# Optimization experiments

Measured on AMD Instinct MI355X. Metric: run time of the kernel, lower is better.

The kernel has to match this reference:

```python
import jax, jax.numpy as jnp
import numpy as np

B, LQ, LK, E, H, NF, NE, HID = 4, 8192, 8192, 256, 8, 2, 4, 256


def _split(x, h):
    b, l, e = x.shape
    return x.reshape(b, l, h, e // h).transpose(0, 2, 1, 3)  # (B,H,L,D)


def _merge(x):
    b, h, l, d = x.shape
    return x.transpose(0, 2, 1, 3).reshape(b, l, h * d)


def _experts(x, W1, b1, W2, b2, W3, b3):
    # x: (B,N,in); W*: (E, out, in). Returns (E,B,N,out). Exact (erf) GELU as torch.
    h = jax.nn.gelu(jnp.einsum('bni,ehi->ebnh', x, W1) + b1[:, None, None, :], approximate=False)
    h = jax.nn.gelu(jnp.einsum('ebnh,egh->ebng', h, W2) + b2[:, None, None, :], approximate=False)
    return jnp.einsum('ebng,eog->ebno', h, W3) + b3[:, None, None, :]


def _combine(expert_out, scores):
    # expert_out: (E,B,N,out); scores: (B,N,1,E) -> (B,N,out)
    return jnp.einsum('ebno,bne->bno', expert_out, scores[:, :, 0, :])


def _forward(scores, query, input_functions,
             ca_Wq, ca_bq, ca_Wk, ca_bk, ca_Wv, ca_bv, ca_Wo, ca_bo,
             sa_Wq, sa_bq, sa_Wk, sa_bk, sa_Wv, sa_bv, sa_Wo, sa_bo,
             f1_W1, f1_b1, f1_W2, f1_b2, f1_W3, f1_b3,
             f2_W1, f2_b1, f2_W2, f2_b2, f2_W3, f2_b3):
    h = H
    # ---- cross attention over NF input functions ----
    q = jax.nn.softmax(_split(query @ ca_Wq.T + ca_bq, h), -1)  # (B,H,Lq,D)
    k = jnp.einsum('fble,fde->fbld', input_functions, ca_Wk) + ca_bk[:, None, None, :]
    v = jnp.einsum('fble,fde->fbld', input_functions, ca_Wv) + ca_bv[:, None, None, :]
    f, b, lk, e = k.shape
    d = e // h
    k = jax.nn.softmax(k.reshape(f, b, lk, h, d).transpose(0, 1, 3, 2, 4), -1)  # (F,B,H,Lk,D)
    v = v.reshape(f, b, lk, h, d).transpose(0, 1, 3, 2, 4)
    k_sum = k.sum(3, keepdims=True)                       # (F,B,H,1,D)
    alpha = 1.0 / (q[None] * k_sum).sum(-1, keepdims=True)  # (F,B,H,Lq,1)
    tmp = jnp.einsum('fbhld,fbhlv->fbhdv', k, v)          # (F,B,H,D,D)
    out = (alpha * jnp.einsum('bhld,fbhdv->fbhlv', q, tmp)).mean(0)  # (B,H,Lq,D)
    ca = (_merge(q) + _merge(out)) @ ca_Wo.T + ca_bo
    # expert FFN1 + score-weighted combine, residual
    query = query + _combine(_experts(ca, f1_W1, f1_b1, f1_W2, f1_b2, f1_W3, f1_b3), scores)
    # ---- self attention ----
    q2 = jax.nn.softmax(_split(query @ sa_Wq.T + sa_bq, h), -1)
    k2 = jax.nn.softmax(_split(query @ sa_Wk.T + sa_bk, h), -1)
    v2 = _split(query @ sa_Wv.T + sa_bv, h)
    k_sum2 = k2.sum(2, keepdims=True)
    alpha2 = 1.0 / (q2 * k_sum2).sum(-1, keepdims=True)
    tmp2 = jnp.einsum('bhld,bhlv->bhdv', k2, v2)
    out2 = alpha2 * jnp.einsum('bhld,bhdv->bhlv', q2, tmp2)
    sa = (_merge(q2) + _merge(out2)) @ sa_Wo.T + sa_bo
    query = query + _combine(_experts(sa, f2_W1, f2_b1, f2_W2, f2_b2, f2_W3, f2_b3), scores)
    return query


def setup_inputs() -> dict:
    ks = iter(jax.random.split(jax.random.key(0), 64))
    def p(shape):
        return jax.random.normal(next(ks), shape, jnp.float32) * 0.02
    inp = {
        'scores': jax.random.uniform(next(ks), (B, LQ, 1, NE), jnp.float32),
        'query': jax.random.normal(next(ks), (B, LQ, E), jnp.float32),
        'input_functions': jax.random.normal(next(ks), (NF, B, LK, E), jnp.float32),
        'ca_Wq': p((E, E)), 'ca_bq': p((E,)),
        'ca_Wk': p((NF, E, E)), 'ca_bk': p((NF, E)),
        'ca_Wv': p((NF, E, E)), 'ca_bv': p((NF, E)),
        'ca_Wo': p((E, E)), 'ca_bo': p((E,)),
        'sa_Wq': p((E, E)), 'sa_bq': p((E,)),
        'sa_Wk': p((E, E)), 'sa_bk': p((E,)),
        'sa_Wv': p((E, E)), 'sa_bv': p((E,)),
        'sa_Wo': p((E, E)), 'sa_bo': p((E,)),
        'f1_W1': p((NE, HID, E)), 'f1_b1': p((NE, HID)),
        'f1_W2': p((NE, HID, HID)), 'f1_b2': p((NE, HID)),
        'f1_W3': p((NE, HID, HID)), 'f1_b3': p((NE, HID)),
        'f2_W1': p((NE, HID, E)), 'f2_b1': p((NE, HID)),
        'f2_W2': p((NE, HID, HID)), 'f2_b2': p((NE, HID)),
        'f2_W3': p((NE, HID, HID)), 'f2_b3': p((NE, HID)),
    }
    return inp


def reference(scores, query, input_functions,
              ca_Wq, ca_bq, ca_Wk, ca_bk, ca_Wv, ca_bv, ca_Wo, ca_bo,
              sa_Wq, sa_bq, sa_Wk, sa_bk, sa_Wv, sa_bv, sa_Wo, sa_bo,
              f1_W1, f1_b1, f1_W2, f1_b2, f1_W3, f1_b3,
              f2_W1, f2_b1, f2_W2, f2_b2, f2_W3, f2_b3):
    return _forward(scores, query, input_functions,
                    ca_Wq, ca_bq, ca_Wk, ca_bk, ca_Wv, ca_bv, ca_Wo, ca_bo,
                    sa_Wq, sa_bq, sa_Wk, sa_bk, sa_Wv, sa_bv, sa_Wo, sa_bo,
                    f1_W1, f1_b1, f1_W2, f1_b2, f1_W3, f1_b3,
                    f2_W1, f2_b1, f2_W2, f2_b2, f2_W3, f2_b3)
```

## Files before the change

kernel.cpp:

```cpp
#include <hip/hip_runtime.h>


typedef unsigned short u16;
typedef __attribute__((ext_vector_type(8))) short   bs8;
typedef __attribute__((ext_vector_type(4))) float   f32x4;
typedef __attribute__((ext_vector_type(16))) float  f32x16;

__device__ __forceinline__ float bf2f(u16 u) {
  union { float f; unsigned i; } c; c.i = ((unsigned)u) << 16; return c.f;
}
__device__ __forceinline__ u16 f2bf(float f) {
  union { float f; unsigned i; } c; c.f = f;
  unsigned x = c.i;
  return (u16)((x + 0x7fffu + ((x >> 16) & 1u)) >> 16);
}
__device__ __forceinline__ unsigned pack2(float a, float b) {
  return (unsigned)f2bf(a) | ((unsigned)f2bf(b) << 16);
}
__device__ __forceinline__ float gelu_f(float x) {
  const float t = x * (0.7978845608f + 0.0356774081f * x * x);
  return x * __builtin_amdgcn_rcpf(1.f + __expf(-2.f * t));
}

#define EPI_PLAIN 0
#define EPI_QSM   4

template <bool AF32, int EPI>
__global__ __launch_bounds__(256, 2) void gemm256(
    const void* __restrict__ Ain, const u16* __restrict__ W,
    const float* __restrict__ bias, u16* __restrict__ outb) {
  __shared__ int4 ash[1024];
  __shared__ int4 wsh[1024];
  const int tid = threadIdx.x;
  const int m0 = blockIdx.x * 128, n0 = blockIdx.y * 128;
  const int wave = tid >> 6, lane = tid & 63;
  const int wm = (wave >> 1) * 64, wn = (wave & 1) * 64;
  const int lr = lane & 15, lk = lane >> 4;
  f32x4 acc[4][4];
#pragma unroll
  for (int m = 0; m < 4; ++m)
#pragma unroll
    for (int n = 0; n < 4; ++n) acc[m][n] = f32x4{0.f, 0.f, 0.f, 0.f};

  const float* Af = (const float*)Ain;
  const u16*   Ab = (const u16*)Ain;

  for (int kt = 0; kt < 4; ++kt) {
    const int k0 = kt * 64;
    if (kt) __syncthreads();
#pragma unroll
    for (int it = 0; it < 4; ++it) {
      const int s = tid + it * 256;
      const int row = s >> 3, c16 = s & 7;
      const int dst = (row << 3) | (c16 ^ (row & 7));
      const long src = (long)(m0 + row) * 256 + k0 + c16 * 8;
      int4 val;
      if constexpr (AF32) {
        const float4* p = (const float4*)(Af + src);
        const float4 x = p[0], y = p[1];
        val.x = pack2(x.x, x.y); val.y = pack2(x.z, x.w);
        val.z = pack2(y.x, y.y); val.w = pack2(y.z, y.w);
      } else {
        val = *(const int4*)(Ab + src);
      }
      ash[dst] = val;
    }
#pragma unroll
    for (int it = 0; it < 4; ++it) {
      const int s = tid + it * 256;
      const int row = s >> 3, c16 = s & 7;
      const int dst = (row << 3) | (c16 ^ (row & 7));
      wsh[dst] = *(const int4*)(W + (long)(n0 + row) * 256 + k0 + c16 * 8);
    }
    __syncthreads();
#pragma unroll
    for (int kk = 0; kk < 2; ++kk) {
      bs8 af[4], wf[4];
#pragma unroll
      for (int m = 0; m < 4; ++m) {
        const int row = wm + m * 16 + lr;
        af[m] = *(const bs8*)&ash[(row << 3) | ((kk * 4 + lk) ^ (row & 7))];
      }
#pragma unroll
      for (int n = 0; n < 4; ++n) {
        const int row = wn + n * 16 + lr;
        wf[n] = *(const bs8*)&wsh[(row << 3) | ((kk * 4 + lk) ^ (row & 7))];
      }
#pragma unroll
      for (int m = 0; m < 4; ++m)
#pragma unroll
        for (int n = 0; n < 4; ++n)
          acc[m][n] = __builtin_amdgcn_mfma_f32_16x16x32_bf16(af[m], wf[n],
                                                              acc[m][n], 0, 0, 0);
    }
  }
  if constexpr (EPI == EPI_QSM) {
#pragma unroll
    for (int m = 0; m < 4; ++m) {
      const int rb = m0 + wm + m * 16 + lk * 4;
#pragma unroll
      for (int j = 0; j < 4; ++j) {
#pragma unroll
        for (int hh = 0; hh < 2; ++hh) {
          const int c0 = n0 + wn + (2 * hh) * 16 + lr;
          const float p0 = __expf(acc[m][2 * hh][j] + bias[c0]);
          const float p1 = __expf(acc[m][2 * hh + 1][j] + bias[c0 + 16]);
          float s = p0 + p1;
#pragma unroll
          for (int o = 8; o >= 1; o >>= 1) s += __shfl_xor(s, o);
          const float inv = 1.0f / s;
          outb[(long)(rb + j) * 256 + c0]      = f2bf(p0 * inv);
          outb[(long)(rb + j) * 256 + c0 + 16] = f2bf(p1 * inv);
        }
      }
    }
  } else {
#pragma unroll
    for (int m = 0; m < 4; ++m) {
      const int rb = m0 + wm + m * 16 + lk * 4;
#pragma unroll
      for (int n = 0; n < 4; ++n) {
        const int gc = n0 + wn + n * 16 + lr;
        const float bv = bias[gc];
#pragma unroll
        for (int j = 0; j < 4; ++j)
          outb[(long)(rb + j) * 256 + gc] = f2bf(acc[m][n][j] + bv);
      }
    }
  }
}

__global__ __launch_bounds__(1024, 4) void ffn4(
    const u16* __restrict__ X, const u16* __restrict__ WX, int wbase,
    const float* __restrict__ b1, const float* __restrict__ b2,
    const float* __restrict__ b3, const float* __restrict__ scores,
    const float* __restrict__ csrc, float* __restrict__ outf) {
  __shared__ int4 xsh[2048];
  __shared__ int4 hsh[2048];
  const int tid = threadIdx.x, wave = tid >> 6, lane = tid & 63;
  const int wm = (wave >> 3) * 32;
  const int wn8 = wave & 7;
  const int lr = lane & 15, lk = lane >> 4;
  const long m0 = (long)blockIdx.x * 64;

#pragma unroll
  for (int it = 0; it < 2; ++it) {
    const int s = tid + it * 1024;
    const int row = s >> 5, c8 = s & 31;
    const int cs = (c8 & 24) | ((c8 ^ row) & 7);
    xsh[row * 32 + cs] = *(const int4*)(X + (m0 + row) * 256 + c8 * 8);
  }
  __syncthreads();

  f32x4 oacc[2][2];
#pragma unroll
  for (int m = 0; m < 2; ++m)
#pragma unroll
    for (int n = 0; n < 2; ++n) oacc[m][n] = f32x4{0.f, 0.f, 0.f, 0.f};
  f32x4 acc[2][2];

  for (int e = 0; e < 4; ++e) {
#pragma unroll 1
    for (int l = 0; l < 3; ++l) {
      const u16* wp = WX + (long)(wbase + l * 4 + e) * 65536 + (long)lane * 8;
      const int4* asrc = (l == 0) ? xsh : hsh;
#pragma unroll
      for (int m = 0; m < 2; ++m)
#pragma unroll
        for (int n = 0; n < 2; ++n) acc[m][n] = f32x4{0.f, 0.f, 0.f, 0.f};
#pragma unroll
      for (int kt = 0; kt < 8; ++kt) {
        bs8 af[2], wf[2];
        const int c8 = kt * 4 + lk;
#pragma unroll
        for (int m = 0; m < 2; ++m) {
          const int row = wm + m * 16 + lr;
          const int cs = (c8 & 24) | ((c8 ^ row) & 7);
          af[m] = *(const bs8*)&asrc[row * 32 + cs];
        }
#pragma unroll
        for (int n = 0; n < 2; ++n)
          wf[n] = *(const bs8*)(wp + ((kt * 16 + wn8 * 2 + n) << 9));
        __builtin_amdgcn_s_setprio(1);
#pragma unroll
        for (int m = 0; m < 2; ++m)
#pragma unroll
          for (int n = 0; n < 2; ++n)
            acc[m][n] = __builtin_amdgcn_mfma_f32_16x16x32_bf16(
                af[m], wf[n], acc[m][n], 0, 0, 0);
        __builtin_amdgcn_s_setprio(0);
      }
      if (l < 2) {
        __syncthreads();
        const float* bb = (l == 0 ? b1 : b2) + e * 256;
        u16* hp = (u16*)hsh;
#pragma unroll
        for (int m = 0; m < 2; ++m)
#pragma unroll
          for (int n = 0; n < 2; ++n) {
            const int col = wn8 * 32 + n * 16 + lr;
            const float bv = bb[col];
            const int c8w = col >> 3;
#pragma unroll
            for (int j = 0; j < 4; ++j) {
              const int row = wm + m * 16 + lk * 4 + j;
              const int cs = (c8w & 24) | ((c8w ^ row) & 7);
              hp[row * 256 + cs * 8 + (col & 7)] =
                  f2bf(gelu_f(acc[m][n][j] + bv));
            }
          }
        __syncthreads();
      } else {
#pragma unroll
        for (int m = 0; m < 2; ++m) {
#pragma unroll
          for (int j = 0; j < 4; ++j) {
            const float sc = scores[(m0 + wm + m * 16 + lk * 4 + j) * 4 + e];
#pragma unroll
            for (int n = 0; n < 2; ++n)
              oacc[m][n][j] +=
                  sc * (acc[m][n][j] + b3[e * 256 + wn8 * 32 + n * 16 + lr]);
          }
        }
      }
    }
  }
#pragma unroll
  for (int m = 0; m < 2; ++m) {
#pragma unroll
    for (int n = 0; n < 2; ++n) {
      const int col = wn8 * 32 + n * 16 + lr;
#pragma unroll
      for (int j = 0; j < 4; ++j) {
        const long idx = (m0 + wm + m * 16 + lk * 4 + j) * 256 + col;
        outf[idx] = csrc[idx] + oacc[m][n][j];
      }
    }
  }
}

__global__ __launch_bounds__(1024, 4) void kvstats(
    const float* __restrict__ Ain, const u16* __restrict__ Wk,
    const u16* __restrict__ Wv, const float* __restrict__ bk,
    const float* __restrict__ bv, float* __restrict__ pks,
    float* __restrict__ ptm) {
  __shared__ __align__(16) char smem[73728];
  int4* ash  = (int4*)smem;
  int4* wksh = ash + 512;
  int4* wvsh = wksh + 2048;
  u16* KnT = (u16*)smem;
  u16* VT  = KnT + 256 * 72;
  const int tid = threadIdx.x;
  const int wave = tid >> 6, lane = tid & 63;
  const int lr = lane & 15, lk = lane >> 4;
  const int kvsel = wave >> 3, w3 = wave & 7;
  const int wm = (w3 >> 2) * 32, wn = (w3 & 3) * 64;
  const int b = blockIdx.y, ch = blockIdx.x;
  const long r0 = (long)b * 8192 + (long)ch * 64;

  f32x4 acc[2][4];
#pragma unroll
  for (int m = 0; m < 2; ++m)
#pragma unroll
    for (int n = 0; n < 4; ++n) acc[m][n] = f32x4{0.f, 0.f, 0.f, 0.f};

  for (int kt = 0; kt < 4; ++kt) {
    const int k0 = kt * 64;
    if (kt) __syncthreads();
    if (tid < 512) {
      const int row = tid >> 3, c16 = tid & 7;
      const int dst = (row << 3) | (c16 ^ (row & 7));
      const float4* p = (const float4*)(Ain + (r0 + row) * 256 + k0 + c16 * 8);
      const float4 x = p[0], y = p[1];
      int4 val;
      val.x = pack2(x.x, x.y); val.y = pack2(x.z, x.w);
      val.z = pack2(y.x, y.y); val.w = pack2(y.z, y.w);
      ash[dst] = val;
    }
#pragma unroll
    for (int it = 0; it < 2; ++it) {
      const int s = tid + it * 1024;
      const int row = s >> 3, c16 = s & 7;
      const int dst = (row << 3) | (c16 ^ (row & 7));
      wksh[dst] = *(const int4*)(Wk + (long)row * 256 + k0 + c16 * 8);
      wvsh[dst] = *(const int4*)(Wv + (long)row * 256 + k0 + c16 * 8);
    }
    __syncthreads();
    const int4* wsh = kvsel ? wvsh : wksh;
#pragma unroll
    for (int kk = 0; kk < 2; ++kk) {
      bs8 af[2], wf[4];
#pragma unroll
      for (int m = 0; m < 2; ++m) {
        const int row = wm + m * 16 + lr;
        af[m] = *(const bs8*)&ash[(row << 3) | ((kk * 4 + lk) ^ (row & 7))];
      }
#pragma unroll
      for (int n = 0; n < 4; ++n) {
        const int row = wn + n * 16 + lr;
        wf[n] = *(const bs8*)&wsh[(row << 3) | ((kk * 4 + lk) ^ (row & 7))];
      }
#pragma unroll
      for (int m = 0; m < 2; ++m)
#pragma unroll
        for (int n = 0; n < 4; ++n)
          acc[m][n] = __builtin_amdgcn_mfma_f32_16x16x32_bf16(af[m], wf[n],
                                                              acc[m][n], 0, 0, 0);
    }
  }
  __syncthreads();

  const float* bias = kvsel ? bv : bk;
  if (kvsel == 0) {
#pragma unroll
    for (int m = 0; m < 2; ++m)
#pragma unroll
      for (int j = 0; j < 4; ++j)
#pragma unroll
        for (int hh = 0; hh < 2; ++hh) {
          const int c0 = wn + (2 * hh) * 16 + lr;
          const float p0 = __expf(acc[m][2 * hh][j] + bias[c0]);
          const float p1 = __expf(acc[m][2 * hh + 1][j] + bias[c0 + 16]);
          float s = p0 + p1;
#pragma unroll
          for (int o = 8; o >= 1; o >>= 1) s += __shfl_xor(s, o);
          const float inv = 1.0f / s;
          acc[m][2 * hh][j] = p0 * inv;
          acc[m][2 * hh + 1][j] = p1 * inv;
        }
  }
  {
    u16* T = kvsel ? VT : KnT;
#pragma unroll
    for (int m = 0; m < 2; ++m) {
      const int rb = wm + m * 16 + lk * 4;
#pragma unroll
      for (int n = 0; n < 4; ++n) {
        const int col = wn + n * 16 + lr;
        float v0 = acc[m][n][0], v1 = acc[m][n][1];
        float v2 = acc[m][n][2], v3 = acc[m][n][3];
        if (kvsel) {
          const float bb = bias[col];
          v0 += bb; v1 += bb; v2 += bb; v3 += bb;
        }
        uint2 w;
        w.x = pack2(v0, v1); w.y = pack2(v2, v3);
        *(uint2*)(T + col * 72 + rb) = w;
      }
    }
  }
  __syncthreads();

  if (kvsel == 0) {
    const int h = w3;
    f32x16 aT, aK;
#pragma unroll
    for (int r = 0; r < 16; ++r) { aT[r] = 0.f; aK[r] = 0.f; }
    bs8 ones;
#pragma unroll
    for (int e = 0; e < 8; ++e) ones[e] = (short)0x3F80;
    const u16* kcol = KnT + (h * 32 + (lane & 31)) * 72;
    const u16* vcol = VT  + (h * 32 + (lane & 31)) * 72;
    const int hi8 = (lane >> 5) * 8;
#pragma unroll
    for (int ks = 0; ks < 4; ++ks) {
      const bs8 a  = *(const bs8*)(kcol + ks * 16 + hi8);
      const bs8 vb = *(const bs8*)(vcol + ks * 16 + hi8);
      aT = __builtin_amdgcn_mfma_f32_32x32x16_bf16(vb, a, aT, 0, 0, 0);
      aK = __builtin_amdgcn_mfma_f32_32x32x16_bf16(a, ones, aK, 0, 0, 0);
    }
    const long blk = (long)b * gridDim.x + ch;
    float* po = ptm + blk * 8192 + h * 1024;
#pragma unroll
    for (int r = 0; r < 16; ++r) {
      const int dv = (r & 3) + 8 * (r >> 2) + 4 * (lane >> 5);
      po[dv * 32 + (lane & 31)] = aT[r];
    }
    if ((lane & 31) == 0) {
#pragma unroll
      for (int r = 0; r < 16; ++r) {
        const int dk = (r & 3) + 8 * (r >> 2) + 4 * (lane >> 5);
        pks[blk * 256 + h * 32 + dk] = aK[r];
      }
    }
  }
}

__global__ void reduceStats(const float* __restrict__ pk,
                            const float* __restrict__ pt,
                            float* __restrict__ ksum, float* __restrict__ tmp) {
  const int b = blockIdx.y;
  const int i = blockIdx.x * 256 + threadIdx.x;
  float s = 0.f;
  if (i < 256) {
    const float* p = pk + (long)b * 128 * 256 + i;
    for (int c = 0; c < 128; ++c) s += p[c * 256];
    ksum[(long)b * 256 + i] = s;
  } else {
    const int j = i - 256;
    const float* p = pt + (long)b * 128 * 8192 + j;
    for (int c = 0; c < 128; ++c) s += p[c * 8192];
    tmp[(long)b * 8192 + j] = s;
  }
}

template <int F>
__global__ __launch_bounds__(256, 2) void mixk(const u16* __restrict__ q,
                                               const float* __restrict__ ksum,
                                               const float* __restrict__ tmp,
                                               u16* __restrict__ out) {
  constexpr int LF = (F == 2) ? 1 : 0;
  constexpr int QS = 264;
  __shared__ u16 qsh[64 * QS];
  __shared__ float alsh[64][17];
  __shared__ float ksh[8][F * 36];
  const int t = threadIdx.x;
  const int h = t >> 5, dv = t & 31;
  const int b = blockIdx.y;
  const long row0 = (long)b * 8192 + (long)blockIdx.x * 64;

#pragma unroll
  for (int it = 0; it < 8; ++it) {
    const int i = t + it * 256;
    const int r = i >> 5, c = i & 31;
    *(int4*)&qsh[r * QS + c * 8] = *(const int4*)&q[(row0 + r) * 256 + c * 8];
  }
#pragma unroll
  for (int f = 0; f < F; ++f)
    ksh[h][f * 36 + dv] = ksum[((long)f * 4 + b) * 256 + t];
  float tr[F][32];
#pragma unroll
  for (int f = 0; f < F; ++f) {
    const float* tp = tmp + ((long)f * 4 + b) * 8192 + h * 1024 + dv * 32;
#pragma unroll
    for (int c = 0; c < 8; ++c) {
      const float4 v = *(const float4*)(tp + c * 4);
      tr[f][c * 4] = v.x; tr[f][c * 4 + 1] = v.y;
      tr[f][c * 4 + 2] = v.z; tr[f][c * 4 + 3] = v.w;
    }
  }
  __syncthreads();

  for (int d = t; d < 64 * 8 * F; d += 256) {
    const int f = d & (F - 1);
    const int hh = (d >> LF) & 7;
    const int r = d >> (3 + LF);
    const u16* qp = &qsh[r * QS + hh * 32];
    const float* kp = &ksh[hh][f * 36];
    float s = 0.f;
#pragma unroll
    for (int c = 0; c < 4; ++c) {
      const bs8 qa = *(const bs8*)(qp + c * 8);
#pragma unroll
      for (int j = 0; j < 8; ++j) s += bf2f((u16)qa[j]) * kp[c * 8 + j];
    }
    alsh[r][(hh << LF) | f] = 1.0f / s;
  }
  __syncthreads();

#pragma unroll 2
  for (int r = 0; r < 64; ++r) {
    float qr[32];
    const u16* qp = &qsh[r * QS + h * 32];
#pragma unroll
    for (int c = 0; c < 4; ++c) {
      const bs8 qa = *(const bs8*)(qp + c * 8);
#pragma unroll
      for (int j = 0; j < 8; ++j) qr[c * 8 + j] = bf2f((u16)qa[j]);
    }
    float acc = 0.f;
#pragma unroll
    for (int f = 0; f < F; ++f) {
      float s0 = 0.f, s1 = 0.f;
#pragma unroll
      for (int dk = 0; dk < 32; dk += 2) {
        s0 += qr[dk] * tr[f][dk];
        s1 += qr[dk + 1] * tr[f][dk + 1];
      }
      acc += (s0 + s1) * alsh[r][(h << LF) | f];
    }
    const float qv = bf2f(qsh[r * QS + t]);
    out[(row0 + r) * 256 + t] = f2bf(qv + acc * (1.0f / (float)F));
  }
}

struct WTab10 { const float* p[10]; };
__global__ void convW(WTab10 tab, u16* __restrict__ dst) {
  const int s = blockIdx.y;
  const long i = ((long)blockIdx.x * 256 + threadIdx.x) * 4;
  const float4 v = *(const float4*)(tab.p[s] + i);
  ushort4 o;
  o.x = f2bf(v.x); o.y = f2bf(v.y); o.z = f2bf(v.z); o.w = f2bf(v.w);
  *(ushort4*)(dst + (long)s * 65536 + i) = o;
}

struct WTab24 { const float* p[24]; };
__global__ void convWX(WTab24 tab, u16* __restrict__ dst) {
  const int s = blockIdx.y;
  const int o8 = blockIdx.x * 256 + threadIdx.x;
  const int kt = o8 >> 10, nt = (o8 >> 6) & 15, lane = o8 & 63;
  const int row = nt * 16 + (lane & 15);
  const int col = kt * 32 + (lane >> 4) * 8;
  const float* src = tab.p[s] + row * 256 + col;
  const float4 a = *(const float4*)src;
  const float4 b = *(const float4*)(src + 4);
  int4 val;
  val.x = pack2(a.x, a.y); val.y = pack2(a.z, a.w);
  val.z = pack2(b.x, b.y); val.w = pack2(b.z, b.w);
  *(int4*)(dst + (long)s * 65536 + (long)o8 * 8) = val;
}

extern "C" void kernel_launch(void* const* d_in, const int* in_sizes, int n_in,
                              void* d_out, int out_size, void* d_ws, size_t ws_size,
                              hipStream_t stream) {
  (void)in_sizes; (void)n_in; (void)out_size; (void)ws_size;
  const float* scores = (const float*)d_in[0];
  const float* query  = (const float*)d_in[1];
  const float* IF     = (const float*)d_in[2];
  const float* ca_Wq = (const float*)d_in[3];  const float* ca_bq = (const float*)d_in[4];
  const float* ca_Wk = (const float*)d_in[5];  const float* ca_bk = (const float*)d_in[6];
  const float* ca_Wv = (const float*)d_in[7];  const float* ca_bv = (const float*)d_in[8];
  const float* ca_Wo = (const float*)d_in[9];  const float* ca_bo = (const float*)d_in[10];
  const float* sa_Wq = (const float*)d_in[11]; const float* sa_bq = (const float*)d_in[12];
  const float* sa_Wk = (const float*)d_in[13]; const float* sa_bk = (const float*)d_in[14];
  const float* sa_Wv = (const float*)d_in[15]; const float* sa_bv = (const float*)d_in[16];
  const float* sa_Wo = (const float*)d_in[17]; const float* sa_bo = (const float*)d_in[18];
  const float* f1W1 = (const float*)d_in[19]; const float* f1b1 = (const float*)d_in[20];
  const float* f1W2 = (const float*)d_in[21]; const float* f1b2 = (const float*)d_in[22];
  const float* f1W3 = (const float*)d_in[23]; const float* f1b3 = (const float*)d_in[24];
  const float* f2W1 = (const float*)d_in[25]; const float* f2b1 = (const float*)d_in[26];
  const float* f2W2 = (const float*)d_in[27]; const float* f2b2 = (const float*)d_in[28];
  const float* f2W3 = (const float*)d_in[29]; const float* f2b3 = (const float*)d_in[30];

  char* ws = (char*)d_ws;
  u16* X0 = (u16*)(ws);
  u16* X1 = (u16*)(ws + 16777216);
  u16* X2 = (u16*)(ws + 33554432);
  float* ptmX3 = (float*)(ws + 50331648);
  u16* W16 = (u16*)(ws + 67108864);
  u16* WX  = (u16*)(ws + 68419584);
  float* ksum = (float*)(ws + 71565312);
  float* tmpb = (float*)(ws + 71573504);
  float* pks  = (float*)(ws + 71835648);
  float* qacc = (float*)d_out;

  WTab10 tab;
  tab.p[0] = ca_Wq; tab.p[1] = ca_Wk; tab.p[2] = ca_Wk + 65536;
  tab.p[3] = ca_Wv; tab.p[4] = ca_Wv + 65536; tab.p[5] = ca_Wo;
  tab.p[6] = sa_Wq; tab.p[7] = sa_Wk; tab.p[8] = sa_Wv; tab.p[9] = sa_Wo;
  convW<<<dim3(64, 10), 256, 0, stream>>>(tab, W16);

  WTab24 tabx;
  for (int e = 0; e < 4; ++e) {
    tabx.p[0 + e]  = f1W1 + e * 65536;
    tabx.p[4 + e]  = f1W2 + e * 65536;
    tabx.p[8 + e]  = f1W3 + e * 65536;
    tabx.p[12 + e] = f2W1 + e * 65536;
    tabx.p[16 + e] = f2W2 + e * 65536;
    tabx.p[20 + e] = f2W3 + e * 65536;
  }
  convWX<<<dim3(32, 24), 256, 0, stream>>>(tabx, WX);

  const dim3 gg(256, 2), gb(256);
  const dim3 kvg(128, 4), kvb(1024);
  gemm256<true, EPI_QSM><<<gg, gb, 0, stream>>>(query, W16 + 0 * 65536L, ca_bq, X0);
  for (int f = 0; f < 2; ++f) {
    kvstats<<<kvg, kvb, 0, stream>>>(IF + (long)f * 8388608,
                                     W16 + (1 + f) * 65536L, W16 + (3 + f) * 65536L,
                                     ca_bk + f * 256, ca_bv + f * 256, pks, ptmX3);
    reduceStats<<<dim3(33, 4), 256, 0, stream>>>(pks, ptmX3, ksum + f * 4 * 256, tmpb + (long)f * 4 * 8192);
  }
  mixk<2><<<dim3(128, 4), 256, 0, stream>>>(X0, ksum, tmpb, X1);
  gemm256<false, EPI_PLAIN><<<gg, gb, 0, stream>>>(X1, W16 + 5 * 65536L, ca_bo, X2);
  ffn4<<<512, 1024, 0, stream>>>(X2, WX, 0, f1b1, f1b2, f1b3, scores, query, qacc);
  gemm256<true, EPI_QSM><<<gg, gb, 0, stream>>>(qacc, W16 + 6 * 65536L, sa_bq, X0);
  kvstats<<<kvg, kvb, 0, stream>>>(qacc, W16 + 7 * 65536L, W16 + 8 * 65536L,
                                   sa_bk, sa_bv, pks, ptmX3);
  reduceStats<<<dim3(33, 4), 256, 0, stream>>>(pks, ptmX3, ksum, tmpb);
  mixk<1><<<dim3(128, 4), 256, 0, stream>>>(X0, ksum, tmpb, X1);
  gemm256<false, EPI_PLAIN><<<gg, gb, 0, stream>>>(X1, W16 + 9 * 65536L, sa_bo, X2);
  ffn4<<<512, 1024, 0, stream>>>(X2, WX, 12, f2b1, f2b2, f2b3, scores, qacc, qacc);
}
```

Before: 419.1 us.

## Halve GEMM row tile and batch both cross-attention KV-stat passes into one launch

The projection GEMM now uses 64-row tiles with 4 blocks per CU instead of 128-row tiles with 2, which doubles the grid and raises occupancy at the cost of less reuse of the weight tile. The two per-function kvstats/reduceStats launches for cross attention are merged into a single launch over a doubled grid, with per-block selection of inputs and weights. This removes two launches and a serialization point between the functions. The partial buffer moves to a larger workspace region that aliases X1, which is safe only if X1 is not live during kvstats. reduceStats must also handle the doubled y dimension correctly.

```diff
diff --git a/kernel.cpp b/kernel.cpp
--- a/kernel.cpp
+++ b/kernel.cpp
@@ -26,19 +26,19 @@
 #define EPI_QSM   4
 
 template <bool AF32, int EPI>
-__global__ __launch_bounds__(256, 2) void gemm256(
+__global__ __launch_bounds__(256, 4) void gemm256(
     const void* __restrict__ Ain, const u16* __restrict__ W,
     const float* __restrict__ bias, u16* __restrict__ outb) {
-  __shared__ int4 ash[1024];
+  __shared__ int4 ash[512];
   __shared__ int4 wsh[1024];
   const int tid = threadIdx.x;
-  const int m0 = blockIdx.x * 128, n0 = blockIdx.y * 128;
+  const int m0 = blockIdx.x * 64, n0 = blockIdx.y * 128;
   const int wave = tid >> 6, lane = tid & 63;
-  const int wm = (wave >> 1) * 64, wn = (wave & 1) * 64;
+  const int wm = (wave >> 1) * 32, wn = (wave & 1) * 64;
   const int lr = lane & 15, lk = lane >> 4;
-  f32x4 acc[4][4];
-#pragma unroll
-  for (int m = 0; m < 4; ++m)
+  f32x4 acc[2][4];
+#pragma unroll
+  for (int m = 0; m < 2; ++m)
 #pragma unroll
     for (int n = 0; n < 4; ++n) acc[m][n] = f32x4{0.f, 0.f, 0.f, 0.f};
 
@@ -49,7 +49,7 @@
     const int k0 = kt * 64;
     if (kt) __syncthreads();
 #pragma unroll
-    for (int it = 0; it < 4; ++it) {
+    for (int it = 0; it < 2; ++it) {
       const int s = tid + it * 256;
       const int row = s >> 3, c16 = s & 7;
       const int dst = (row << 3) | (c16 ^ (row & 7));
@@ -75,9 +75,9 @@
     __syncthreads();
 #pragma unroll
     for (int kk = 0; kk < 2; ++kk) {
-      bs8 af[4], wf[4];
-#pragma unroll
-      for (int m = 0; m < 4; ++m) {
+      bs8 af[2], wf[4];
+#pragma unroll
+      for (int m = 0; m < 2; ++m) {
         const int row = wm + m * 16 + lr;
         af[m] = *(const bs8*)&ash[(row << 3) | ((kk * 4 + lk) ^ (row & 7))];
       }
@@ -87,7 +87,7 @@
         wf[n] = *(const bs8*)&wsh[(row << 3) | ((kk * 4 + lk) ^ (row & 7))];
       }
 #pragma unroll
-      for (int m = 0; m < 4; ++m)
+      for (int m = 0; m < 2; ++m)
 #pragma unroll
         for (int n = 0; n < 4; ++n)
           acc[m][n] = __builtin_amdgcn_mfma_f32_16x16x32_bf16(af[m], wf[n],
@@ -96,7 +96,7 @@
   }
   if constexpr (EPI == EPI_QSM) {
 #pragma unroll
-    for (int m = 0; m < 4; ++m) {
+    for (int m = 0; m < 2; ++m) {
       const int rb = m0 + wm + m * 16 + lk * 4;
 #pragma unroll
       for (int j = 0; j < 4; ++j) {
@@ -116,7 +116,7 @@
     }
   } else {
 #pragma unroll
-    for (int m = 0; m < 4; ++m) {
+    for (int m = 0; m < 2; ++m) {
       const int rb = m0 + wm + m * 16 + lk * 4;
 #pragma unroll
       for (int n = 0; n < 4; ++n) {
@@ -240,10 +240,12 @@
 }
 
 __global__ __launch_bounds__(1024, 4) void kvstats(
-    const float* __restrict__ Ain, const u16* __restrict__ Wk,
-    const u16* __restrict__ Wv, const float* __restrict__ bk,
-    const float* __restrict__ bv, float* __restrict__ pks,
-    float* __restrict__ ptm) {
+    const float* __restrict__ A0, const float* __restrict__ A1,
+    const u16* __restrict__ Wk0, const u16* __restrict__ Wk1,
+    const u16* __restrict__ Wv0, const u16* __restrict__ Wv1,
+    const float* __restrict__ bk0, const float* __restrict__ bk1,
+    const float* __restrict__ bv0, const float* __restrict__ bv1,
+    float* __restrict__ pks, float* __restrict__ ptm) {
   __shared__ __align__(16) char smem[73728];
   int4* ash  = (int4*)smem;
   int4* wksh = ash + 512;
@@ -255,7 +257,13 @@
   const int lr = lane & 15, lk = lane >> 4;
   const int kvsel = wave >> 3, w3 = wave & 7;
   const int wm = (w3 >> 2) * 32, wn = (w3 & 3) * 64;
-  const int b = blockIdx.y, ch = blockIdx.x;
+  const int fb = blockIdx.y, ch = blockIdx.x;
+  const int f = fb >> 2, b = fb & 3;
+  const float* Ain = f ? A1 : A0;
+  const u16* Wk = f ? Wk1 : Wk0;
+  const u16* Wv = f ? Wv1 : Wv0;
+  const float* bk = f ? bk1 : bk0;
+  const float* bv = f ? bv1 : bv0;
   const long r0 = (long)b * 8192 + (long)ch * 64;
 
   f32x4 acc[2][4];
@@ -369,7 +377,7 @@
       aT = __builtin_amdgcn_mfma_f32_32x32x16_bf16(vb, a, aT, 0, 0, 0);
       aK = __builtin_amdgcn_mfma_f32_32x32x16_bf16(a, ones, aK, 0, 0, 0);
     }
-    const long blk = (long)b * gridDim.x + ch;
+    const long blk = (long)fb * gridDim.x + ch;
     float* po = ptm + blk * 8192 + h * 1024;
 #pragma unroll
     for (int r = 0; r < 16; ++r) {
@@ -536,7 +544,7 @@
   u16* X0 = (u16*)(ws);
   u16* X1 = (u16*)(ws + 16777216);
   u16* X2 = (u16*)(ws + 33554432);
-  float* ptmX3 = (float*)(ws + 50331648);
+  float* ptmBig = (float*)(ws + 16777216);
   u16* W16 = (u16*)(ws + 67108864);
   u16* WX  = (u16*)(ws + 68419584);
   float* ksum = (float*)(ws + 71565312);
@@ -561,22 +569,22 @@
   }
   convWX<<<dim3(32, 24), 256, 0, stream>>>(tabx, WX);
 
-  const dim3 gg(256, 2), gb(256);
-  const dim3 kvg(128, 4), kvb(1024);
+  const dim3 gg(512, 2), gb(256);
   gemm256<true, EPI_QSM><<<gg, gb, 0, stream>>>(query, W16 + 0 * 65536L, ca_bq, X0);
-  for (int f = 0; f < 2; ++f) {
-    kvstats<<<kvg, kvb, 0, stream>>>(IF + (long)f * 8388608,
-                                     W16 + (1 + f) * 65536L, W16 + (3 + f) * 65536L,
-                                     ca_bk + f * 256, ca_bv + f * 256, pks, ptmX3);
-    reduceStats<<<dim3(33, 4), 256, 0, stream>>>(pks, ptmX3, ksum + f * 4 * 256, tmpb + (long)f * 4 * 8192);
-  }
+  kvstats<<<dim3(128, 8), 1024, 0, stream>>>(
+      IF, IF + 8388608L,
+      W16 + 1 * 65536L, W16 + 2 * 65536L, W16 + 3 * 65536L, W16 + 4 * 65536L,
+      ca_bk, ca_bk + 256, ca_bv, ca_bv + 256, pks, ptmBig);
+  reduceStats<<<dim3(33, 8), 256, 0, stream>>>(pks, ptmBig, ksum, tmpb);
   mixk<2><<<dim3(128, 4), 256, 0, stream>>>(X0, ksum, tmpb, X1);
   gemm256<false, EPI_PLAIN><<<gg, gb, 0, stream>>>(X1, W16 + 5 * 65536L, ca_bo, X2);
   ffn4<<<512, 1024, 0, stream>>>(X2, WX, 0, f1b1, f1b2, f1b3, scores, query, qacc);
   gemm256<true, EPI_QSM><<<gg, gb, 0, stream>>>(qacc, W16 + 6 * 65536L, sa_bq, X0);
-  kvstats<<<kvg, kvb, 0, stream>>>(qacc, W16 + 7 * 65536L, W16 + 8 * 65536L,
-                                   sa_bk, sa_bv, pks, ptmX3);
-  reduceStats<<<dim3(33, 4), 256, 0, stream>>>(pks, ptmX3, ksum, tmpb);
+  kvstats<<<dim3(128, 4), 1024, 0, stream>>>(
+      qacc, qacc,
+      W16 + 7 * 65536L, W16 + 7 * 65536L, W16 + 8 * 65536L, W16 + 8 * 65536L,
+      sa_bk, sa_bk, sa_bv, sa_bv, pks, ptmBig);
+  reduceStats<<<dim3(33, 4), 256, 0, stream>>>(pks, ptmBig, ksum, tmpb);
   mixk<1><<<dim3(128, 4), 256, 0, stream>>>(X0, ksum, tmpb, X1);
   gemm256<false, EPI_PLAIN><<<gg, gb, 0, stream>>>(X1, W16 + 9 * 65536L, sa_bo, X2);
   ffn4<<<512, 1024, 0, stream>>>(X2, WX, 12, f2b1, f2b2, f2b3, scores, qacc, qacc);
```

After: 415.1 us. Within noise of the previous version (-1.0%).
